# Performance work log

Measured on AMD Instinct MI355X. Metric: run time of the kernel, lower is better.

## Reference

```python
import jax, jax.numpy as jnp
import numpy as np
import math

B, T, C = 4, 2048, 2048
H, D = 16, 128
DH = D // 2  # 64 rotation planes
OMEGA_SCALE = 16.0
EPS = 1e-5


def setup_inputs() -> dict:
    key = jax.random.key(0)
    ks = jax.random.split(key, 8)
    w_std = 1.0 / math.sqrt(C)
    x = jax.random.normal(ks[0], (B, T, C), dtype=jnp.float32)
    Wq = jax.random.normal(ks[1], (C, C), dtype=jnp.float32) * w_std
    Wk = jax.random.normal(ks[2], (C, C), dtype=jnp.float32) * w_std
    Wv = jax.random.normal(ks[3], (C, C), dtype=jnp.float32) * w_std
    # c_proj init std = 0.5/sqrt(n_embd)/sqrt(n_layer), n_layer=24
    Wo = jax.random.normal(ks[4], (C, C), dtype=jnp.float32) * (0.5 / math.sqrt(C) / math.sqrt(24))
    # omega_proj: weight init zeros, bias = softplus_inverse(0.001); perturb weight slightly for a nontrivial phase
    w_omega = jax.random.normal(ks[5], (1, C), dtype=jnp.float32) * 0.01
    b_omega = jnp.full((1,), math.log(math.expm1(0.001)), dtype=jnp.float32)
    # log_freq initialized from RoPE inverse frequencies, base 10000
    inv_freq = 1.0 / (10000.0 ** (np.arange(0, D, 2, dtype=np.float32) / D))
    log_freq = jnp.asarray(np.log(inv_freq), dtype=jnp.float32)
    q_gamma = jnp.ones((D,), dtype=jnp.float32)
    k_gamma = jnp.ones((D,), dtype=jnp.float32)
    return {"x": x, "Wq": Wq, "Wk": Wk, "Wv": Wv, "Wo": Wo,
            "w_omega": w_omega, "b_omega": b_omega, "log_freq": log_freq,
            "q_gamma": q_gamma, "k_gamma": k_gamma}


def _rmsnorm(t, gamma):
    return t * jax.lax.rsqrt(jnp.mean(t * t, axis=-1, keepdims=True) + EPS) * gamma


def reference(x, Wq, Wk, Wv, Wo, w_omega, b_omega, log_freq, q_gamma, k_gamma):
    # cumulative contextual phase: omega = sigmoid(omega_proj(x)/scale); phi_t = sum_{tau<t} omega_tau
    omega = jax.nn.sigmoid((x @ w_omega.T + b_omega).astype(jnp.float32) / OMEGA_SCALE)  # (B,T,1)
    phi = jnp.cumsum(omega, axis=1) - omega                                              # (B,T,1)

    q = (x @ Wq.T).reshape(B, T, H, D)
    k = (x @ Wk.T).reshape(B, T, H, D)
    v = (x @ Wv.T).reshape(B, T, H, D)

    # shared-across-heads frequencies theta_j; angles (B,T,1,DH) broadcast over heads
    freq = jnp.exp(log_freq)                       # (DH,)
    angles = phi[..., None] * freq                 # (B,T,1,DH)
    cos = jnp.cos(angles)
    sin = jnp.sin(angles)

    def rotate(t):
        t1, t2 = t[..., :DH], t[..., DH:]
        return jnp.concatenate([t1 * cos + t2 * sin, -t1 * sin + t2 * cos], axis=-1)

    q = rotate(q)
    k = rotate(k)
    q = _rmsnorm(q, q_gamma)
    k = _rmsnorm(k, k_gamma)

    # causal SDPA, scale 1/sqrt(D)
    scores = jnp.einsum('bthd,bshd->bhts', q, k) / math.sqrt(D)   # (B,H,T,T)
    mask = jnp.tril(jnp.ones((T, T), dtype=bool))
    scores = jnp.where(mask, scores, jnp.finfo(scores.dtype).min)
    probs = jax.nn.softmax(scores, axis=-1)
    y = jnp.einsum('bhts,bshd->bthd', probs, v)                   # (B,T,H,D)
    return y.reshape(B, T, H * D) @ Wo.T
```

## Files before the change

### kernel.cpp

```cpp
#include <hip/hip_runtime.h>
#include <math.h>

typedef __bf16 bf16;
typedef __bf16 bf16x8 __attribute__((ext_vector_type(8)));
typedef __bf16 bf16x4v __attribute__((ext_vector_type(4)));
typedef float f32x4 __attribute__((ext_vector_type(4)));

#define NB 4
#define NT 2048
#define NC 2048
#define NH 16
#define ND 128
#define NROW (NB*NT)

#define GLD16(g, l) __builtin_amdgcn_global_load_lds( \
    (__attribute__((address_space(1))) void*)(g), \
    (__attribute__((address_space(3))) void*)(l), 16, 0, 0)

__global__ void cvtx_omega_kernel(const float* __restrict__ x, bf16* __restrict__ xb,
                                  const float* __restrict__ w_om, const float* __restrict__ b_om,
                                  float* __restrict__ omega) {
  int row = blockIdx.x;
  const float4* xr = reinterpret_cast<const float4*>(x + (size_t)row * NC);
  const float4* wr = reinterpret_cast<const float4*>(w_om);
  bf16x4v* ob = reinterpret_cast<bf16x4v*>(xb + (size_t)row * NC);
  float sum = 0.f;
  for (int i = threadIdx.x; i < NC/4; i += 256) {
    float4 a = xr[i], b = wr[i];
    sum += a.x*b.x + a.y*b.y + a.z*b.z + a.w*b.w;
    bf16x4v o;
    o[0] = (bf16)a.x; o[1] = (bf16)a.y; o[2] = (bf16)a.z; o[3] = (bf16)a.w;
    ob[i] = o;
  }
  for (int m = 32; m; m >>= 1) sum += __shfl_xor(sum, m);
  __shared__ float wsum[4];
  if ((threadIdx.x & 63) == 0) wsum[threadIdx.x >> 6] = sum;
  __syncthreads();
  if (threadIdx.x == 0) {
    float d = wsum[0] + wsum[1] + wsum[2] + wsum[3] + b_om[0];
    omega[row] = 1.f / (1.f + expf(-d * (1.f/16.f)));
  }
}

__global__ void cvtw_kernel(const float* __restrict__ W0, const float* __restrict__ W1,
                            const float* __restrict__ W2, const float* __restrict__ W3,
                            bf16* __restrict__ o0, bf16* __restrict__ o1,
                            bf16* __restrict__ o2, bf16* __restrict__ o3) {
  int which = blockIdx.x >> 12;
  const float* in = which == 0 ? W0 : which == 1 ? W1 : which == 2 ? W2 : W3;
  bf16* out = which == 0 ? o0 : which == 1 ? o1 : which == 2 ? o2 : o3;
  int i = (blockIdx.x & 4095) * 256 + threadIdx.x;
  float4 v = reinterpret_cast<const float4*>(in)[i];
  bf16x4v o;
  o[0] = (bf16)v.x; o[1] = (bf16)v.y; o[2] = (bf16)v.z; o[3] = (bf16)v.w;
  reinterpret_cast<bf16x4v*>(out)[i] = o;
}

__global__ void scan_kernel(const float* __restrict__ omega, float* __restrict__ phi) {
  int b = blockIdx.x;
  const float* om = omega + (size_t)b * NT;
  float* ph = phi + (size_t)b * NT;
  int t = threadIdx.x;
  float v[8]; float s = 0.f;
  #pragma unroll
  for (int j = 0; j < 8; j++) { v[j] = om[t*8 + j]; s += v[j]; }
  __shared__ float totals[256];
  __shared__ double base_sh[256];
  totals[t] = s;
  __syncthreads();
  if (t == 0) {
    double run = 0.0;
    for (int i = 0; i < 256; i++) { base_sh[i] = run; run += (double)totals[i]; }
  }
  __syncthreads();
  double run = base_sh[t];
  #pragma unroll
  for (int j = 0; j < 8; j++) { ph[t*8 + j] = (float)run; run += (double)v[j]; }
}

__global__ void sincos_kernel(const float* __restrict__ phi, const float* __restrict__ log_freq,
                              float* __restrict__ cos_t, float* __restrict__ sin_t) {
  int i = blockIdx.x * 256 + threadIdx.x;
  int row = i >> 6, dd = i & 63;
  float f = expf(log_freq[dd]);
  float a = phi[row] * f;
  float si, co;
  sincosf(a, &si, &co);
  cos_t[i] = co;
  sin_t[i] = si;
}

template<int MODE>
__global__ __launch_bounds__(512, 2)
void gemm256(const bf16* __restrict__ Ag, const bf16* __restrict__ Bg,
             void* __restrict__ Cout,
             const float* __restrict__ cos_t, const float* __restrict__ sin_t,
             const float* __restrict__ gamma, float outscale) {
  constexpr int NKT = NC / 64;
  __shared__ bf16 Als[2][256 * 64];
  __shared__ bf16 Bls[2][256 * 64];
  const int t = threadIdx.x;
  const int lane = t & 63, lg = lane >> 4, l15 = lane & 15;
  const int wid = t >> 6, wm = wid >> 1, wn = wid & 1;
  const int bid = blockIdx.x;
  const int wg = (bid & 7) * 32 + (bid >> 3);
  const int m0 = (wg >> 3) * 256, n0 = (wg & 7) * 256;

  const size_t K2 = (size_t)NC * 2;
  const int scol = ((t & 7) * 16) ^ (((t >> 3) & 7) << 4);
  const char* aS = (const char*)Ag + (size_t)(m0 + (t >> 3)) * K2 + scol;
  const char* bS = (const char*)Bg + (size_t)(n0 + (t >> 3)) * K2 + scol;

  const int colk0 = (lg * 16) ^ ((l15 & 7) << 4);
  const int colk[2] = { colk0, colk0 ^ 64 };
  const int arow = (wm * 64 + l15) * 128;
  const int brow = (wn * 128 + l15) * 128;

  f32x4 acc[4][8] = {};

#define STAGE_TA(kt, d) do { \
    const char* sa_ = aS + (size_t)(kt) * 128; \
    char* da_ = (char*)&Als[d][0] + t * 16; \
    GLD16(sa_,            da_); \
    GLD16(sa_ +  64*K2,   da_ + 8192); \
    GLD16(sa_ + 128*K2,   da_ + 16384); \
    GLD16(sa_ + 192*K2,   da_ + 24576); \
  } while(0)
#define STAGE_TB(kt, d) do { \
    const char* sb_ = bS + (size_t)(kt) * 128; \
    char* db_ = (char*)&Bls[d][0] + t * 16; \
    GLD16(sb_,            db_); \
    GLD16(sb_ +  64*K2,   db_ + 8192); \
    GLD16(sb_ + 128*K2,   db_ + 16384); \
    GLD16(sb_ + 192*K2,   db_ + 24576); \
  } while(0)

  STAGE_TA(0, 0); STAGE_TB(0, 0);
  asm volatile("s_waitcnt vmcnt(0)" ::: "memory");
  __builtin_amdgcn_s_barrier();
  asm volatile("" ::: "memory");

  bf16x8 aC[2][2], bC[4][2];
  for (int kt = 0; kt < NKT; kt++) {
    const int d = kt & 1;
    const char* Ab = (const char*)&Als[d][0];
    const char* Bb = (const char*)&Bls[d][0];
    const bool pf = (kt + 1 < NKT);

    #pragma unroll
    for (int i = 0; i < 2; i++)
      #pragma unroll
      for (int kk = 0; kk < 2; kk++)
        aC[i][kk] = *(const bf16x8*)(Ab + arow + (i*16)*128 + colk[kk]);
    #pragma unroll
    for (int j = 0; j < 4; j++)
      #pragma unroll
      for (int kk = 0; kk < 2; kk++)
        bC[j][kk] = *(const bf16x8*)(Bb + brow + (j*16)*128 + colk[kk]);
    if (pf) STAGE_TA(kt+1, d^1);
    __builtin_amdgcn_s_barrier();
    asm volatile("s_waitcnt lgkmcnt(0)");
    __builtin_amdgcn_s_setprio(1);
    #pragma unroll
    for (int kk = 0; kk < 2; kk++)
      #pragma unroll
      for (int i = 0; i < 2; i++)
        #pragma unroll
        for (int j = 0; j < 4; j++)
          acc[i][j] = __builtin_amdgcn_mfma_f32_16x16x32_bf16(aC[i][kk], bC[j][kk], acc[i][j], 0,0,0);
    __builtin_amdgcn_s_setprio(0);

    #pragma unroll
    for (int i = 0; i < 2; i++)
      #pragma unroll
      for (int kk = 0; kk < 2; kk++)
        aC[i][kk] = *(const bf16x8*)(Ab + arow + ((32 + i*16))*128 + colk[kk]);
    if (pf) STAGE_TB(kt+1, d^1);
    __builtin_amdgcn_s_barrier();
    asm volatile("s_waitcnt lgkmcnt(0)");
    __builtin_amdgcn_s_setprio(1);
    #pragma unroll
    for (int kk = 0; kk < 2; kk++)
      #pragma unroll
      for (int i = 0; i < 2; i++)
        #pragma unroll
        for (int j = 0; j < 4; j++)
          acc[2+i][j] = __builtin_amdgcn_mfma_f32_16x16x32_bf16(aC[i][kk], bC[j][kk], acc[2+i][j], 0,0,0);
    __builtin_amdgcn_s_setprio(0);

    #pragma unroll
    for (int j = 0; j < 4; j++)
      #pragma unroll
      for (int kk = 0; kk < 2; kk++)
        bC[j][kk] = *(const bf16x8*)(Bb + brow + ((64 + j*16))*128 + colk[kk]);
    __builtin_amdgcn_s_barrier();
    asm volatile("s_waitcnt lgkmcnt(0)");
    __builtin_amdgcn_s_setprio(1);
    #pragma unroll
    for (int kk = 0; kk < 2; kk++)
      #pragma unroll
      for (int i = 0; i < 2; i++)
        #pragma unroll
        for (int j = 0; j < 4; j++)
          acc[2+i][4+j] = __builtin_amdgcn_mfma_f32_16x16x32_bf16(aC[i][kk], bC[j][kk], acc[2+i][4+j], 0,0,0);
    __builtin_amdgcn_s_setprio(0);

    #pragma unroll
    for (int i = 0; i < 2; i++)
      #pragma unroll
      for (int kk = 0; kk < 2; kk++)
        aC[i][kk] = *(const bf16x8*)(Ab + arow + (i*16)*128 + colk[kk]);
    __builtin_amdgcn_s_barrier();
    asm volatile("s_waitcnt lgkmcnt(0)");
    __builtin_amdgcn_s_setprio(1);
    #pragma unroll
    for (int kk = 0; kk < 2; kk++)
      #pragma unroll
      for (int i = 0; i < 2; i++)
        #pragma unroll
        for (int j = 0; j < 4; j++)
          acc[i][4+j] = __builtin_amdgcn_mfma_f32_16x16x32_bf16(aC[i][kk], bC[j][kk], acc[i][4+j], 0,0,0);
    __builtin_amdgcn_s_setprio(0);

    asm volatile("s_waitcnt vmcnt(0)" ::: "memory");
    __builtin_amdgcn_s_barrier();
    asm volatile("" ::: "memory");
  }
#undef STAGE_TA
#undef STAGE_TB

  if constexpr (MODE == 0) {
    bf16* out = (bf16*)Cout;
    #pragma unroll
    for (int mi = 0; mi < 4; mi++) {
      #pragma unroll
      for (int r = 0; r < 4; r++) {
        int m = m0 + wm*64 + mi*16 + lg*4 + r;
        float ss = 0.f;
        #pragma unroll
        for (int nj = 0; nj < 8; nj++) { float v = acc[mi][nj][r]; ss += v*v; }
        ss += __shfl_xor(ss, 1); ss += __shfl_xor(ss, 2);
        ss += __shfl_xor(ss, 4); ss += __shfl_xor(ss, 8);
        float scale = rsqrtf(ss * (1.f/128.f) + 1e-5f) * outscale;
        size_t rowb = (size_t)m * NC + n0 + wn*128;
        size_t tabb = (size_t)m * 64;
        #pragma unroll
        for (int nj = 0; nj < 4; nj++) {
          int dd = nj*16 + l15;
          float c = cos_t[tabb + dd];
          float s = sin_t[tabb + dd];
          float t1 = acc[mi][nj][r], t2 = acc[mi][nj+4][r];
          float o1 = (t1*c + t2*s) * scale * gamma[dd];
          float o2 = (t2*c - t1*s) * scale * gamma[dd + 64];
          out[rowb + dd] = (bf16)o1;
          out[rowb + dd + 64] = (bf16)o2;
        }
      }
    }
  } else if constexpr (MODE == 1) {
    bf16* vt = (bf16*)Cout;
    const int h = (n0 + wn*128) >> 7;
    #pragma unroll
    for (int mi = 0; mi < 4; mi++) {
      #pragma unroll
      for (int r = 0; r < 4; r++) {
        int m = m0 + wm*64 + mi*16 + lg*4 + r;
        int bidx = m >> 11, tt = m & (NT-1);
        size_t hb = (((size_t)bidx * NH + h) * ND) * NT + tt;
        #pragma unroll
        for (int nj = 0; nj < 8; nj++) {
          int d = nj*16 + l15;
          vt[hb + (size_t)d * NT] = (bf16)acc[mi][nj][r];
        }
      }
    }
  } else {
    float* out = (float*)Cout;
    #pragma unroll
    for (int mi = 0; mi < 4; mi++) {
      #pragma unroll
      for (int r = 0; r < 4; r++) {
        int m = m0 + wm*64 + mi*16 + lg*4 + r;
        size_t rowb = (size_t)m * NC + n0 + wn*128;
        #pragma unroll
        for (int nj = 0; nj < 8; nj++)
          out[rowb + nj*16 + l15] = acc[mi][nj][r];
      }
    }
  }
}

__global__ __launch_bounds__(512, 2)
void fa_kernel(const bf16* __restrict__ Qg, const bf16* __restrict__ Kg,
               const bf16* __restrict__ Vt, bf16* __restrict__ Og) {
  __shared__ bf16 Kls[2][64 * 128];
  __shared__ bf16 Vls[2][128 * 64];
  __shared__ bf16 Pls[8][32 * 64];
  const int t = threadIdx.x, w = t >> 6, lane = t & 63, lg = lane >> 4, l15 = lane & 15;
  const int bh = blockIdx.x;
  const int qb = (gridDim.y - 1) - blockIdx.y;
  const size_t qkbase = (size_t)(bh >> 4) * NT * NC + (size_t)(bh & 15) * ND;
  const size_t vbase  = (size_t)bh * ND * NT;
  const int q0 = qb * 256 + w * 32;

  bf16x8 qf[2][4];
  #pragma unroll
  for (int mt = 0; mt < 2; mt++)
    #pragma unroll
    for (int kc = 0; kc < 4; kc++)
      qf[mt][kc] = *reinterpret_cast<const bf16x8*>(
          Qg + qkbase + (size_t)(q0 + mt*16 + l15) * NC + kc*32 + lg*8);

  f32x4 oacc[2][8] = {};
  f32x4 lacc[2] = {};
  float m_run[2][4];
  #pragma unroll
  for (int mt = 0; mt < 2; mt++)
    #pragma unroll
    for (int r = 0; r < 4; r++) m_run[mt][r] = -1e30f;

  bf16x8 vone;
  #pragma unroll
  for (int i = 0; i < 8; i++) vone[i] = (bf16)1.0f;

  const int kinS = ((t & 15) * 16) ^ (((t >> 4) & 7) << 4);
  const char* ksrc0 = (const char*)(Kg + qkbase) + (size_t)(t >> 4) * (NC*2) + kinS;
  const int vinS = ((t & 7) * 16) ^ (((t >> 3) & 7) << 4);
  const char* vsrc0 = (const char*)(Vt + vbase) + (size_t)(t >> 3) * (NT*2) + vinS;

#define STAGE_KV(kt, dd) do { \
    const char* ks_ = ksrc0 + (size_t)(kt) * 64 * (NC*2); \
    const char* vs_ = vsrc0 + (size_t)(kt) * 128; \
    char* kd_ = (char*)&Kls[dd][0] + t * 16; \
    char* vd_ = (char*)&Vls[dd][0] + t * 16; \
    GLD16(ks_,                        kd_); \
    GLD16(ks_ + (size_t)32 * NC * 2,  kd_ + 8192); \
    GLD16(vs_,                        vd_); \
    GLD16(vs_ + (size_t)64 * NT * 2,  vd_ + 8192); \
  } while(0)

  const int ntiles = 4 * qb + 4;
  STAGE_KV(0, 0);
  asm volatile("s_waitcnt vmcnt(0)" ::: "memory");
  __builtin_amdgcn_s_barrier();
  asm volatile("" ::: "memory");

  for (int kt = 0; kt < ntiles; kt++) {
    const int d = kt & 1;
    const int kv0 = kt * 64;
    if (kt + 1 < ntiles) STAGE_KV(kt + 1, d ^ 1);

    if (q0 + 31 >= kv0) {
      f32x4 s[2][4] = {};
      __builtin_amdgcn_s_setprio(1);
      #pragma unroll
      for (int kc = 0; kc < 4; kc++) {
        bf16x8 kf[4];
        const int swz = ((kc*64 + lg*16) ^ ((l15 & 7) << 4));
        #pragma unroll
        for (int nt = 0; nt < 4; nt++)
          kf[nt] = *reinterpret_cast<const bf16x8*>((const char*)&Kls[d][0] + (nt*16 + l15) * 256 + swz);
        #pragma unroll
        for (int mt = 0; mt < 2; mt++)
          #pragma unroll
          for (int nt = 0; nt < 4; nt++)
            s[mt][nt] = __builtin_amdgcn_mfma_f32_16x16x32_bf16(qf[mt][kc], kf[nt], s[mt][nt], 0, 0, 0);
      }
      __builtin_amdgcn_s_setprio(0);

      if (kv0 + 63 > q0) {
        #pragma unroll
        for (int mt = 0; mt < 2; mt++)
          #pragma unroll
          for (int nt = 0; nt < 4; nt++) {
            int kv = kv0 + nt*16 + l15;
            #pragma unroll
            for (int r = 0; r < 4; r++)
              if (kv > q0 + mt*16 + lg*4 + r) s[mt][nt][r] = -1e30f;
          }
      }

      float tmax[2][4];
      #pragma unroll
      for (int mt = 0; mt < 2; mt++)
        #pragma unroll
        for (int r = 0; r < 4; r++) {
          float tm = fmaxf(fmaxf(s[mt][0][r], s[mt][1][r]), fmaxf(s[mt][2][r], s[mt][3][r]));
          tm = fmaxf(tm, __shfl_xor(tm, 1));
          tm = fmaxf(tm, __shfl_xor(tm, 2));
          tm = fmaxf(tm, __shfl_xor(tm, 4));
          tm = fmaxf(tm, __shfl_xor(tm, 8));
          tmax[mt][r] = tm;
        }

      int ok = 1;
      #pragma unroll
      for (int mt = 0; mt < 2; mt++)
        #pragma unroll
        for (int r = 0; r < 4; r++) ok &= (tmax[mt][r] <= m_run[mt][r] + 8.0f);
      if (!__all(ok)) {
        #pragma unroll
        for (int mt = 0; mt < 2; mt++) {
          f32x4 alv;
          #pragma unroll
          for (int r = 0; r < 4; r++) {
            float mn = fmaxf(m_run[mt][r], tmax[mt][r]);
            alv[r] = exp2f(m_run[mt][r] - mn);
            m_run[mt][r] = mn;
          }
          #pragma unroll
          for (int dt = 0; dt < 8; dt++) {
            f32x4 o = oacc[mt][dt];
            o[0] *= alv[0]; o[1] *= alv[1]; o[2] *= alv[2]; o[3] *= alv[3];
            oacc[mt][dt] = o;
          }
          f32x4 lv = lacc[mt];
          lv[0] *= alv[0]; lv[1] *= alv[1]; lv[2] *= alv[2]; lv[3] *= alv[3];
          lacc[mt] = lv;
        }
      }

      char* pw = (char*)&Pls[w][0];
      #pragma unroll
      for (int mt = 0; mt < 2; mt++)
        #pragma unroll
        for (int r = 0; r < 4; r++) {
          float p0 = exp2f(s[mt][0][r] - m_run[mt][r]);
          float p1 = exp2f(s[mt][1][r] - m_run[mt][r]);
          float p2 = exp2f(s[mt][2][r] - m_run[mt][r]);
          float p3 = exp2f(s[mt][3][r] - m_run[mt][r]);
          int qrow = mt*16 + lg*4 + r;
          int rb = qrow * 128, cX = (qrow & 7) << 4;
          *(bf16*)(pw + rb + ((       2*l15) ^ cX)) = (bf16)p0;
          *(bf16*)(pw + rb + (( 32 +  2*l15) ^ cX)) = (bf16)p1;
          *(bf16*)(pw + rb + (( 64 +  2*l15) ^ cX)) = (bf16)p2;
          *(bf16*)(pw + rb + (( 96 +  2*l15) ^ cX)) = (bf16)p3;
        }

      asm volatile("s_waitcnt lgkmcnt(0)" ::: "memory");

      bf16x8 pf[2][2];
      #pragma unroll
      for (int mt = 0; mt < 2; mt++)
        #pragma unroll
        for (int kc2 = 0; kc2 < 2; kc2++)
          pf[mt][kc2] = *reinterpret_cast<const bf16x8*>(
              pw + (mt*16 + l15) * 128 + ((kc2*64 + lg*16) ^ ((l15 & 7) << 4)));
      __builtin_amdgcn_s_setprio(1);
      #pragma unroll
      for (int kc2 = 0; kc2 < 2; kc2++) {
        #pragma unroll
        for (int mt = 0; mt < 2; mt++)
          lacc[mt] = __builtin_amdgcn_mfma_f32_16x16x32_bf16(pf[mt][kc2], vone, lacc[mt], 0, 0, 0);
        const int swz = ((kc2*64 + lg*16) ^ ((l15 & 7) << 4));
        #pragma unroll
        for (int dt = 0; dt < 8; dt++) {
          bf16x8 vf = *reinterpret_cast<const bf16x8*>((const char*)&Vls[d][0] + (dt*16 + l15) * 128 + swz);
          #pragma unroll
          for (int mt = 0; mt < 2; mt++)
            oacc[mt][dt] = __builtin_amdgcn_mfma_f32_16x16x32_bf16(pf[mt][kc2], vf, oacc[mt][dt], 0, 0, 0);
        }
      }
      __builtin_amdgcn_s_setprio(0);
    }

    asm volatile("s_waitcnt vmcnt(0)" ::: "memory");
    __builtin_amdgcn_s_barrier();
    asm volatile("" ::: "memory");
  }
#undef STAGE_KV

  #pragma unroll
  for (int mt = 0; mt < 2; mt++)
    #pragma unroll
    for (int r = 0; r < 4; r++) {
      float inv = 1.f / lacc[mt][r];
      size_t orow = qkbase + (size_t)(q0 + mt*16 + lg*4 + r) * NC;
      #pragma unroll
      for (int dt = 0; dt < 8; dt++)
        Og[orow + dt*16 + l15] = (bf16)(oacc[mt][dt][r] * inv);
    }
}

extern "C" void kernel_launch(void* const* d_in, const int* in_sizes, int n_in,
                              void* d_out, int out_size, void* d_ws, size_t ws_size,
                              hipStream_t stream) {
  (void)in_sizes; (void)n_in; (void)out_size; (void)ws_size;
  const float* x       = (const float*)d_in[0];
  const float* Wq      = (const float*)d_in[1];
  const float* Wk      = (const float*)d_in[2];
  const float* Wv      = (const float*)d_in[3];
  const float* Wo      = (const float*)d_in[4];
  const float* w_omega = (const float*)d_in[5];
  const float* b_omega = (const float*)d_in[6];
  const float* log_freq= (const float*)d_in[7];
  const float* q_gamma = (const float*)d_in[8];
  const float* k_gamma = (const float*)d_in[9];

  char* p = (char*)d_ws;
  auto alloc = [&](size_t bytes) { void* r = (void*)p; p += (bytes + 255) & ~(size_t)255; return r; };
  bf16* xb   = (bf16*)alloc((size_t)NROW * NC * 2);
  bf16* wqb  = (bf16*)alloc((size_t)NC * NC * 2);
  bf16* wkb  = (bf16*)alloc((size_t)NC * NC * 2);
  bf16* wvb  = (bf16*)alloc((size_t)NC * NC * 2);
  bf16* wob  = (bf16*)alloc((size_t)NC * NC * 2);
  bf16* qb   = (bf16*)alloc((size_t)NROW * NC * 2);
  bf16* kb   = (bf16*)alloc((size_t)NROW * NC * 2);
  bf16* vt   = (bf16*)alloc((size_t)NROW * NC * 2);
  bf16* ob   = (bf16*)alloc((size_t)NROW * NC * 2);
  float* omega = (float*)alloc((size_t)NROW * 4);
  float* phi   = (float*)alloc((size_t)NROW * 4);
  float* cos_t = (float*)alloc((size_t)NROW * 64 * 4);
  float* sin_t = (float*)alloc((size_t)NROW * 64 * 4);

  cvtx_omega_kernel<<<NROW, 256, 0, stream>>>(x, xb, w_omega, b_omega, omega);
  cvtw_kernel<<<16384, 256, 0, stream>>>(Wq, Wk, Wv, Wo, wqb, wkb, wvb, wob);
  scan_kernel<<<NB, 256, 0, stream>>>(omega, phi);
  sincos_kernel<<<NROW * 64 / 256, 256, 0, stream>>>(phi, log_freq, cos_t, sin_t);

  const float sc2 = 0.12751726f;
  gemm256<0><<<256, 512, 0, stream>>>(xb, wqb, qb, cos_t, sin_t, q_gamma, sc2);
  gemm256<0><<<256, 512, 0, stream>>>(xb, wkb, kb, cos_t, sin_t, k_gamma, 1.0f);
  gemm256<1><<<256, 512, 0, stream>>>(xb, wvb, vt, nullptr, nullptr, nullptr, 1.0f);

  fa_kernel<<<dim3(NB * NH, NT / 256), 512, 0, stream>>>(qb, kb, vt, ob);

  gemm256<2><<<256, 512, 0, stream>>>(ob, wob, d_out, nullptr, nullptr, nullptr, 1.0f);
}
```

Baseline: 462.8 us.

## Split GEMM LDS tiles into half-tiles and stage loads at finer granularity

Rewrites the 256x256 bf16 GEMM main loop so each LDS buffer holds two independently staged halves of A and B. Global-to-LDS loads for the next k-tiles are issued per half-tile right after each barrier, with partial vmcnt waits instead of a full drain each iteration, and the loop is unrolled over two k-steps. The aim is to keep loads in flight across MFMA phases and remove the per-iteration full-wait stall. The row mapping of the A and B halves changes, so the epilogue's accumulator indexing must still match. The tighter wait schedule also adds a risk of race bugs.

After: 423.4 us. 8.5% less time.

```diff
diff --git a/kernel.cpp b/kernel.cpp
--- a/kernel.cpp
+++ b/kernel.cpp
@@ -96,7 +96,6 @@
              void* __restrict__ Cout,
              const float* __restrict__ cos_t, const float* __restrict__ sin_t,
              const float* __restrict__ gamma, float outscale) {
-  constexpr int NKT = NC / 64;
   __shared__ bf16 Als[2][256 * 64];
   __shared__ bf16 Bls[2][256 * 64];
   const int t = threadIdx.x;
@@ -107,127 +106,96 @@
   const int m0 = (wg >> 3) * 256, n0 = (wg & 7) * 256;
 
   const size_t K2 = (size_t)NC * 2;
-  const int scol = ((t & 7) * 16) ^ (((t >> 3) & 7) << 4);
-  const char* aS = (const char*)Ag + (size_t)(m0 + (t >> 3)) * K2 + scol;
-  const char* bS = (const char*)Bg + (size_t)(n0 + (t >> 3)) * K2 + scol;
+  const int u = t >> 3;
+  const int scol = ((t & 7) * 16) ^ ((u & 7) << 4);
+  const char* a1S = (const char*)Ag + (size_t)(m0 + (u >> 5) * 64 + (u & 31)) * K2 + scol;
+  const char* b1S = (const char*)Bg + (size_t)(n0 + u) * K2 + scol;
 
   const int colk0 = (lg * 16) ^ ((l15 & 7) << 4);
-  const int colk[2] = { colk0, colk0 ^ 64 };
-  const int arow = (wm * 64 + l15) * 128;
-  const int brow = (wn * 128 + l15) * 128;
+  const int colk1 = colk0 ^ 64;
+
+  char* const A0u1 = (char*)&Als[0][0];
+  char* const A0u2 = A0u1 + 16384;
+  char* const A1u1 = (char*)&Als[1][0];
+  char* const A1u2 = A1u1 + 16384;
+  char* const B0u1 = (char*)&Bls[0][0];
+  char* const B0u2 = B0u1 + 16384;
+  char* const B1u1 = (char*)&Bls[1][0];
+  char* const B1u2 = B1u1 + 16384;
 
   f32x4 acc[4][8] = {};
-
-#define STAGE_TA(kt, d) do { \
-    const char* sa_ = aS + (size_t)(kt) * 128; \
-    char* da_ = (char*)&Als[d][0] + t * 16; \
-    GLD16(sa_,            da_); \
-    GLD16(sa_ +  64*K2,   da_ + 8192); \
-    GLD16(sa_ + 128*K2,   da_ + 16384); \
-    GLD16(sa_ + 192*K2,   da_ + 24576); \
-  } while(0)
-#define STAGE_TB(kt, d) do { \
-    const char* sb_ = bS + (size_t)(kt) * 128; \
-    char* db_ = (char*)&Bls[d][0] + t * 16; \
-    GLD16(sb_,            db_); \
-    GLD16(sb_ +  64*K2,   db_ + 8192); \
-    GLD16(sb_ + 128*K2,   db_ + 16384); \
-    GLD16(sb_ + 192*K2,   db_ + 24576); \
-  } while(0)
-
-  STAGE_TA(0, 0); STAGE_TB(0, 0);
-  asm volatile("s_waitcnt vmcnt(0)" ::: "memory");
-  __builtin_amdgcn_s_barrier();
-  asm volatile("" ::: "memory");
-
   bf16x8 aC[2][2], bC[4][2];
-  for (int kt = 0; kt < NKT; kt++) {
-    const int d = kt & 1;
-    const char* Ab = (const char*)&Als[d][0];
-    const char* Bb = (const char*)&Bls[d][0];
-    const bool pf = (kt + 1 < NKT);
-
-    #pragma unroll
-    for (int i = 0; i < 2; i++)
-      #pragma unroll
-      for (int kk = 0; kk < 2; kk++)
-        aC[i][kk] = *(const bf16x8*)(Ab + arow + (i*16)*128 + colk[kk]);
-    #pragma unroll
-    for (int j = 0; j < 4; j++)
-      #pragma unroll
-      for (int kk = 0; kk < 2; kk++)
-        bC[j][kk] = *(const bf16x8*)(Bb + brow + (j*16)*128 + colk[kk]);
-    if (pf) STAGE_TA(kt+1, d^1);
-    __builtin_amdgcn_s_barrier();
-    asm volatile("s_waitcnt lgkmcnt(0)");
-    __builtin_amdgcn_s_setprio(1);
-    #pragma unroll
-    for (int kk = 0; kk < 2; kk++)
-      #pragma unroll
-      for (int i = 0; i < 2; i++)
-        #pragma unroll
-        for (int j = 0; j < 4; j++)
-          acc[i][j] = __builtin_amdgcn_mfma_f32_16x16x32_bf16(aC[i][kk], bC[j][kk], acc[i][j], 0,0,0);
-    __builtin_amdgcn_s_setprio(0);
-
-    #pragma unroll
-    for (int i = 0; i < 2; i++)
-      #pragma unroll
-      for (int kk = 0; kk < 2; kk++)
-        aC[i][kk] = *(const bf16x8*)(Ab + arow + ((32 + i*16))*128 + colk[kk]);
-    if (pf) STAGE_TB(kt+1, d^1);
-    __builtin_amdgcn_s_barrier();
-    asm volatile("s_waitcnt lgkmcnt(0)");
-    __builtin_amdgcn_s_setprio(1);
-    #pragma unroll
-    for (int kk = 0; kk < 2; kk++)
-      #pragma unroll
-      for (int i = 0; i < 2; i++)
-        #pragma unroll
-        for (int j = 0; j < 4; j++)
-          acc[2+i][j] = __builtin_amdgcn_mfma_f32_16x16x32_bf16(aC[i][kk], bC[j][kk], acc[2+i][j], 0,0,0);
-    __builtin_amdgcn_s_setprio(0);
-
-    #pragma unroll
-    for (int j = 0; j < 4; j++)
-      #pragma unroll
-      for (int kk = 0; kk < 2; kk++)
-        bC[j][kk] = *(const bf16x8*)(Bb + brow + ((64 + j*16))*128 + colk[kk]);
-    __builtin_amdgcn_s_barrier();
-    asm volatile("s_waitcnt lgkmcnt(0)");
-    __builtin_amdgcn_s_setprio(1);
-    #pragma unroll
-    for (int kk = 0; kk < 2; kk++)
-      #pragma unroll
-      for (int i = 0; i < 2; i++)
-        #pragma unroll
-        for (int j = 0; j < 4; j++)
-          acc[2+i][4+j] = __builtin_amdgcn_mfma_f32_16x16x32_bf16(aC[i][kk], bC[j][kk], acc[2+i][4+j], 0,0,0);
-    __builtin_amdgcn_s_setprio(0);
-
-    #pragma unroll
-    for (int i = 0; i < 2; i++)
-      #pragma unroll
-      for (int kk = 0; kk < 2; kk++)
-        aC[i][kk] = *(const bf16x8*)(Ab + arow + (i*16)*128 + colk[kk]);
-    __builtin_amdgcn_s_barrier();
-    asm volatile("s_waitcnt lgkmcnt(0)");
-    __builtin_amdgcn_s_setprio(1);
-    #pragma unroll
-    for (int kk = 0; kk < 2; kk++)
-      #pragma unroll
-      for (int i = 0; i < 2; i++)
-        #pragma unroll
-        for (int j = 0; j < 4; j++)
-          acc[i][4+j] = __builtin_amdgcn_mfma_f32_16x16x32_bf16(aC[i][kk], bC[j][kk], acc[i][4+j], 0,0,0);
-    __builtin_amdgcn_s_setprio(0);
-
-    asm volatile("s_waitcnt vmcnt(0)" ::: "memory");
-    __builtin_amdgcn_s_barrier();
-    asm volatile("" ::: "memory");
-  }
-#undef STAGE_TA
-#undef STAGE_TB
+
+#define STG(src, dst, kt) do { \
+    const char* s_ = (src) + (size_t)(kt) * 128; \
+    char* d_ = (dst) + t * 16; \
+    GLD16(s_, d_); GLD16(s_ + (size_t)128 * K2, d_ + 8192); } while(0)
+#define STG_A1(kt, d) STG(a1S, (d) ? A1u1 : A0u1, kt)
+#define STG_A2(kt, d) STG(a1S + (size_t)32 * K2, (d) ? A1u2 : A0u2, kt)
+#define STG_B1(kt, d) STG(b1S, (d) ? B1u1 : B0u1, kt)
+#define STG_B2(kt, d) STG(b1S + (size_t)64 * K2, (d) ? B1u2 : B0u2, kt)
+
+#define RDA(base) do { _Pragma("unroll") \
+    for (int i2 = 0; i2 < 2; i2++) { \
+      const char* p_ = (base) + (wm * 32 + i2 * 16 + l15) * 128; \
+      aC[i2][0] = *(const bf16x8*)(p_ + colk0); \
+      aC[i2][1] = *(const bf16x8*)(p_ + colk1); } } while(0)
+#define RDB(base) do { _Pragma("unroll") \
+    for (int j2 = 0; j2 < 4; j2++) { \
+      const char* p_ = (base) + (wn * 64 + j2 * 16 + l15) * 128; \
+      bC[j2][0] = *(const bf16x8*)(p_ + colk0); \
+      bC[j2][1] = *(const bf16x8*)(p_ + colk1); } } while(0)
+
+#define MM(IB, JB) do { __builtin_amdgcn_s_setprio(1); \
+    _Pragma("unroll") \
+    for (int kk = 0; kk < 2; kk++) \
+      _Pragma("unroll") \
+      for (int i2 = 0; i2 < 2; i2++) \
+        _Pragma("unroll") \
+        for (int j2 = 0; j2 < 4; j2++) \
+          acc[(IB)+i2][(JB)+j2] = __builtin_amdgcn_mfma_f32_16x16x32_bf16(aC[i2][kk], bC[j2][kk], acc[(IB)+i2][(JB)+j2], 0,0,0); \
+    __builtin_amdgcn_s_setprio(0); } while(0)
+
+#define VM(n) asm volatile("s_waitcnt vmcnt(" #n ")" ::: "memory")
+#define BAR() do { __builtin_amdgcn_s_barrier(); asm volatile("" ::: "memory"); } while(0)
+#define LGK() asm volatile("s_waitcnt lgkmcnt(0)" ::: "memory")
+
+  STG_A1(0, 0); STG_A2(0, 0); STG_B1(0, 0); STG_B2(0, 0); STG_B1(1, 1); STG_A2(1, 1);
+  VM(6); BAR();
+
+  #pragma unroll 1
+  for (int i = 0; i < 15; i++) {
+    const int o1 = 2*i + 1, e2 = 2*i + 2, o3 = 2*i + 3;
+    RDA(A0u1); RDB(B0u1);           BAR(); STG_A1(o1, 1); LGK(); MM(0, 0);
+    RDA(A0u2); VM(6);               BAR(); STG_B2(o1, 1); LGK(); MM(2, 0);
+    RDB(B0u2);                      BAR(); STG_B1(e2, 0); LGK(); MM(2, 4);
+    RDA(A0u1); VM(4);               BAR(); STG_A2(e2, 0); LGK(); MM(0, 4);
+    RDA(A1u1); RDB(B1u1);           BAR(); STG_A1(e2, 0); LGK(); MM(0, 0);
+    RDA(A1u2); VM(6);               BAR(); STG_B2(e2, 0); LGK(); MM(2, 0);
+    RDB(B1u2);                      BAR(); STG_B1(o3, 1); LGK(); MM(2, 4);
+    RDA(A1u1); VM(4);               BAR(); STG_A2(o3, 1); LGK(); MM(0, 4);
+  }
+  {
+    RDA(A0u1); RDB(B0u1);           BAR(); STG_A1(31, 1); LGK(); MM(0, 0);
+    RDA(A0u2); VM(6);               BAR(); STG_B2(31, 1); LGK(); MM(2, 0);
+    RDB(B0u2);                      BAR();                LGK(); MM(2, 4);
+    RDA(A0u1); VM(2);               BAR();                LGK(); MM(0, 4);
+    RDA(A1u1); RDB(B1u1);           BAR();                LGK(); MM(0, 0);
+    RDA(A1u2); VM(0);               BAR();                LGK(); MM(2, 0);
+    RDB(B1u2);                      BAR();                LGK(); MM(2, 4);
+    RDA(A1u1);                      BAR();                LGK(); MM(0, 4);
+  }
+#undef STG
+#undef STG_A1
+#undef STG_A2
+#undef STG_B1
+#undef STG_B2
+#undef RDA
+#undef RDB
+#undef MM
+#undef VM
+#undef BAR
+#undef LGK
 
   if constexpr (MODE == 0) {
     bf16* out = (bf16*)Cout;
```
